# Optimization experiments

Hardware: AMD Instinct MI355X
Metric: run time of the kernel (lower is better)

Reference implementation:

```python
import jax, jax.numpy as jnp
import numpy as np

N = 100000   # nodes
E = 1600000  # edges (avg degree 16)
D = 128      # feature / hidden dim


def setup_inputs() -> dict:
    key = jax.random.key(0)
    k_x, k_e, k_w1, k_w2 = jax.random.split(key, 4)
    scale = 1.0 / np.sqrt(D)
    return {
        "x": jax.random.normal(k_x, (N, D), dtype=jnp.float32),
        "W1": jax.random.normal(k_w1, (D, D), dtype=jnp.float32) * scale,
        "b1": jnp.zeros((D,), dtype=jnp.float32),
        "W2": jax.random.normal(k_w2, (D, D), dtype=jnp.float32) * scale,
        "b2": jnp.zeros((D,), dtype=jnp.float32),
        "edge_index": jax.random.randint(k_e, (2, E), 0, N, dtype=jnp.int64),
    }


def _gcn_conv(h, src, dst, norm, W, b, n_nodes):
    # GCNConv: out = scatter_add(norm * (h @ W)[src] -> dst) + b
    y = h @ W                                   # [N, D] dense GEMM
    msgs = y[src] * norm[:, None]               # [E+N, D] gather + scale
    agg = jax.ops.segment_sum(msgs, dst, num_segments=n_nodes)  # scatter-add
    return agg + b


def reference(x, W1, b1, W2, b2, edge_index):
    n_nodes = x.shape[0]
    # add self loops (GCNConv default add_self_loops=True)
    loop = jnp.arange(n_nodes, dtype=edge_index.dtype)
    src = jnp.concatenate([edge_index[0], loop])
    dst = jnp.concatenate([edge_index[1], loop])
    # symmetric normalization: deg over destinations incl. self loops
    deg = jax.ops.segment_sum(jnp.ones_like(src, dtype=x.dtype), dst,
                              num_segments=n_nodes)
    dinv = jnp.where(deg > 0, jax.lax.rsqrt(deg), 0.0)
    norm = dinv[src] * dinv[dst]                # [E+N]
    # dropout in eval mode (identity); layer = conv -> ReLU, twice
    h = jax.nn.relu(_gcn_conv(x, src, dst, norm, W1, b1, n_nodes))
    h = jax.nn.relu(_gcn_conv(h, src, dst, norm, W2, b2, n_nodes))
    return h
```

## Files before the change

kernel.cpp:

```cpp
#include <hip/hip_runtime.h>
#include <hip/hip_bf16.h>


#define DIM 128
#define BSH 9
#define NBKT 196

typedef __attribute__((ext_vector_type(8))) short bf16x8;
typedef __attribute__((ext_vector_type(4))) float f32x4;


__global__ __launch_bounds__(256) void k_bcount(const int* __restrict__ dst,
                                                int E, int* __restrict__ bcnt) {
    __shared__ int h[NBKT];
    int t = threadIdx.x;
    for (int b = t; b < NBKT; b += 256) h[b] = 0;
    __syncthreads();
    for (int e = blockIdx.x * 256 + t; e < E; e += gridDim.x * 256)
        atomicAdd(&h[dst[e] >> BSH], 1);
    __syncthreads();
    for (int b = t; b < NBKT; b += 256)
        if (h[b]) atomicAdd(&bcnt[b], h[b]);
}

__global__ void k_bscan(const int* __restrict__ bcnt, int* __restrict__ bbase,
                        int* __restrict__ bcur) {
    __shared__ int a[256], c[256];
    int t = threadIdx.x;
    int v = (t < NBKT) ? bcnt[t] : 0;
    a[t] = v;
    __syncthreads();
    int* A = a; int* B = c;
    for (int off = 1; off < 256; off <<= 1) {
        B[t] = A[t] + (t >= off ? A[t - off] : 0);
        __syncthreads();
        int* tmp = A; A = B; B = tmp;
    }
    int incl = A[t];
    if (t < NBKT) { int ex = incl - v; bbase[t] = ex; bcur[t] = ex; }
    if (t == NBKT - 1) bbase[NBKT] = incl;
}

__global__ __launch_bounds__(256) void k_bscatter(
    const int* __restrict__ src, const int* __restrict__ dst, int E,
    int* __restrict__ bcur, uint2* __restrict__ out) {
    __shared__ uint2 stage[NBKT * 16];
    __shared__ int scnt[NBKT];
    __shared__ int needflush;
    int t = threadIdx.x;
    for (int b = t; b < NBKT; b += 256) scnt[b] = 0;
    if (t == 0) needflush = 0;
    __syncthreads();

    int per = (E + gridDim.x - 1) / gridDim.x;
    int s0 = blockIdx.x * per;
    int s1 = min(E, s0 + per);

    for (int base = s0; base < s1; base += 1024) {
#pragma unroll
        for (int k = 0; k < 4; ++k) {
            int e = base + t + k * 256;
            if (e < s1) {
                int d = dst[e];
                uint2 pr; pr.x = (uint)d; pr.y = (uint)src[e];
                int b = d >> BSH;
                int slot = atomicAdd(&scnt[b], 1);
                if (slot < 16) {
                    stage[b * 16 + slot] = pr;
                    if (slot == 15) needflush = 1;
                } else {
                    int c = atomicAdd(&bcur[b], 1);
                    out[c] = pr;
                }
            }
        }
        __syncthreads();
        if (needflush) {
            for (int bb = t; bb < NBKT; bb += 256) {
                if (scnt[bb] >= 16) {
                    int cur = atomicAdd(&bcur[bb], 16);
#pragma unroll
                    for (int k = 0; k < 16; ++k) out[cur + k] = stage[bb * 16 + k];
                    scnt[bb] = 0;
                }
            }
            __syncthreads();
            if (t == 0) needflush = 0;
            __syncthreads();
        }
    }
    for (int bb = t; bb < NBKT; bb += 256) {
        int c = scnt[bb]; if (c > 16) c = 16;
        if (c > 0) {
            int cur = atomicAdd(&bcur[bb], c);
            for (int k = 0; k < c; ++k) out[cur + k] = stage[bb * 16 + k];
        }
    }
}

__global__ __launch_bounds__(256) void k_bcsc(
    const uint2* __restrict__ pairs, const int* __restrict__ bbase,
    int* __restrict__ rowptr, float* __restrict__ dinv,
    int* __restrict__ col, int n) {
    __shared__ int lh[512], ls[512];
    int b = blockIdx.x, t = threadIdx.x;
    int p0 = bbase[b], p1 = bbase[b + 1];
    int d0 = b << BSH;

    lh[t] = 0; lh[t + 256] = 0;
    __syncthreads();
    for (int i = p0 + t; i < p1; i += 256)
        atomicAdd(&lh[pairs[i].x & 511], 1);
    __syncthreads();

    int deg0 = lh[t], deg1 = lh[t + 256];
    int* A = lh; int* B = ls;
    for (int off = 1; off < 512; off <<= 1) {
        B[t]       = A[t]       + (t       >= off ? A[t - off]       : 0);
        B[t + 256] = A[t + 256] + (t + 256 >= off ? A[t + 256 - off] : 0);
        __syncthreads();
        int* tmp = A; A = B; B = tmp;
    }
    int ex0 = A[t] - deg0, ex1 = A[t + 256] - deg1;
    __syncthreads();
    B[t] = ex0; B[t + 256] = ex1;

    int nd = d0 + t;
    if (nd < n) { rowptr[nd] = p0 + ex0; dinv[nd] = rsqrtf((float)(deg0 + 1)); }
    nd = d0 + t + 256;
    if (nd < n) { rowptr[nd] = p0 + ex1; dinv[nd] = rsqrtf((float)(deg1 + 1)); }
    if (b == NBKT - 1 && t == 0) rowptr[n] = p1;
    __syncthreads();

    for (int i = p0 + t; i < p1; i += 256) {
        uint2 pr = pairs[i];
        int slot = p0 + atomicAdd(&B[pr.x & 511], 1);
        col[slot] = (int)pr.y;
    }
}


__global__ void k_cast_x(const float* __restrict__ x, ushort* __restrict__ xb,
                         int total4) {
    int i = blockIdx.x * 256 + threadIdx.x;
    if (i < total4) {
        float4 v = ((const float4*)x)[i];
        __hip_bfloat16 a = __float2bfloat16(v.x), b = __float2bfloat16(v.y);
        __hip_bfloat16 c = __float2bfloat16(v.z), d = __float2bfloat16(v.w);
        ushort4 o = make_ushort4(*(ushort*)&a, *(ushort*)&b,
                                 *(ushort*)&c, *(ushort*)&d);
        ((ushort4*)xb)[i] = o;
    }
}

__global__ void k_split_w(const float* __restrict__ W, ushort* __restrict__ Wpk) {
    int idx = blockIdx.x * 256 + threadIdx.x;
    if (idx >= 16384) return;
    int j    = idx & 7;
    int lane = (idx >> 3) & 63;
    int ks   = (idx >> 9) & 3;
    int ct   = idx >> 11;
    int k  = ks * 32 + (lane >> 4) * 8 + j;
    int nn = ct * 16 + (lane & 15);
    float w = W[k * 128 + nn];
    __hip_bfloat16 hi = __float2bfloat16(w);
    float rem = w - __bfloat162float(hi);
    __hip_bfloat16 lo = __float2bfloat16(rem);
    Wpk[idx]         = *(ushort*)&hi;
    Wpk[16384 + idx] = *(ushort*)&lo;
}

__global__ __launch_bounds__(256, 2) void k_gemm_mfma(
    const ushort* __restrict__ xb, const ushort* __restrict__ Wpk,
    const float* __restrict__ dinv, ushort* __restrict__ y,
    int n, int ntiles) {
    __shared__ ushort Wl[32768];
    int t = threadIdx.x;
    {
        const uint4* s4 = (const uint4*)Wpk;
        uint4* d4 = (uint4*)Wl;
#pragma unroll
        for (int i = 0; i < 16; ++i) d4[t + 256 * i] = s4[t + 256 * i];
    }
    __syncthreads();

    const int wave = t >> 6, lane = t & 63;
    const int l15 = lane & 15, lg = lane >> 4;

    for (int tile = blockIdx.x; tile < ntiles; tile += gridDim.x) {
        int row0 = tile * 64 + wave * 16;
        int arow = row0 + l15;
        if (arow >= n) arow = n - 1;
        const ushort* xp = xb + (size_t)arow * 128 + lg * 8;

        bf16x8 a[4];
#pragma unroll
        for (int ks = 0; ks < 4; ++ks)
            a[ks] = *(const bf16x8*)(xp + ks * 32);

        f32x4 acc[8];
#pragma unroll
        for (int ct = 0; ct < 8; ++ct) acc[ct] = (f32x4)(0.f);

#pragma unroll
        for (int ks = 0; ks < 4; ++ks) {
#pragma unroll
            for (int ct = 0; ct < 8; ++ct) {
                bf16x8 b = *(const bf16x8*)&Wl[(size_t)((0 * 8 + ct) * 4 + ks) * 512 + lane * 8];
                acc[ct] = __builtin_amdgcn_mfma_f32_16x16x32_bf16(a[ks], b, acc[ct], 0, 0, 0);
            }
#pragma unroll
            for (int ct = 0; ct < 8; ++ct) {
                bf16x8 b = *(const bf16x8*)&Wl[(size_t)((1 * 8 + ct) * 4 + ks) * 512 + lane * 8];
                acc[ct] = __builtin_amdgcn_mfma_f32_16x16x32_bf16(a[ks], b, acc[ct], 0, 0, 0);
            }
        }

#pragma unroll
        for (int r = 0; r < 4; ++r) {
            int row = row0 + lg * 4 + r;
            if (row < n) {
                float dv = dinv[row];
                ushort* yr = y + (size_t)row * 128 + l15;
#pragma unroll
                for (int ct = 0; ct < 8; ++ct) {
                    __hip_bfloat16 h = __float2bfloat16(acc[ct][r] * dv);
                    yr[ct * 16] = *(ushort*)&h;
                }
            }
        }
    }
}

template <int MODE>
__global__ __launch_bounds__(256) void k_agg2(
    const ushort* __restrict__ yb, const int* __restrict__ rowptr,
    const int* __restrict__ col, const float* __restrict__ dinv,
    const float* __restrict__ bias, void* __restrict__ outp, int n) {
    int t = threadIdx.x, lane = t & 63;
    int node = blockIdx.x * 4 + (t >> 6);
    if (node >= n) return;

    uint v0 = *(const uint*)(yb + (size_t)node * 128 + lane * 2);
    float ax = __uint_as_float(v0 << 16);
    float ay = __uint_as_float(v0 & 0xffff0000u);

    int lo = rowptr[node], hi = rowptr[node + 1];
    int i = lo;
    for (; i + 4 <= hi; i += 4) {
        int s0 = col[i], s1 = col[i + 1], s2 = col[i + 2], s3 = col[i + 3];
        uint w0 = *(const uint*)(yb + (size_t)s0 * 128 + lane * 2);
        uint w1 = *(const uint*)(yb + (size_t)s1 * 128 + lane * 2);
        uint w2 = *(const uint*)(yb + (size_t)s2 * 128 + lane * 2);
        uint w3 = *(const uint*)(yb + (size_t)s3 * 128 + lane * 2);
        ax += __uint_as_float(w0 << 16);         ay += __uint_as_float(w0 & 0xffff0000u);
        ax += __uint_as_float(w1 << 16);         ay += __uint_as_float(w1 & 0xffff0000u);
        ax += __uint_as_float(w2 << 16);         ay += __uint_as_float(w2 & 0xffff0000u);
        ax += __uint_as_float(w3 << 16);         ay += __uint_as_float(w3 & 0xffff0000u);
    }
    for (; i < hi; ++i) {
        int s = col[i];
        uint w = *(const uint*)(yb + (size_t)s * 128 + lane * 2);
        ax += __uint_as_float(w << 16);
        ay += __uint_as_float(w & 0xffff0000u);
    }

    float dv = dinv[node];
    float2 b = ((const float2*)bias)[lane];
    float ox = fmaxf(ax * dv + b.x, 0.f);
    float oy = fmaxf(ay * dv + b.y, 0.f);

    if (MODE == 0) {
        __hip_bfloat16 ha = __float2bfloat16(ox), hb = __float2bfloat16(oy);
        uint o = ((uint)(*(ushort*)&hb) << 16) | (uint)(*(ushort*)&ha);
        ((uint*)outp)[(size_t)node * 64 + lane] = o;
    } else {
        ((float2*)outp)[(size_t)node * 64 + lane] = make_float2(ox, oy);
    }
}


extern "C" void kernel_launch(void* const* d_in, const int* in_sizes, int n_in,
                              void* d_out, int out_size, void* d_ws, size_t ws_size,
                              hipStream_t stream) {
    const float* x  = (const float*)d_in[0];
    const float* W1 = (const float*)d_in[1];
    const float* b1 = (const float*)d_in[2];
    const float* W2 = (const float*)d_in[3];
    const float* b2 = (const float*)d_in[4];
    const int*   ei = (const int*)d_in[5];

    const int n = in_sizes[0] / DIM;
    const int E = in_sizes[5] / 2;
    const int* src = ei;
    const int* dst = ei + E;
    float* out = (float*)d_out;

    char* w = (char*)d_ws;
    ushort* xb    = (ushort*)w;  w += (size_t)n * DIM * sizeof(ushort);
    ushort* h     = (ushort*)w;  w += (size_t)n * DIM * sizeof(ushort);
    uint2*  bpair = (uint2*)w;   w += (size_t)E * sizeof(uint2);
    ushort* wpk1  = (ushort*)w;  w += 32768 * sizeof(ushort);
    ushort* wpk2  = (ushort*)w;  w += 32768 * sizeof(ushort);
    float*  dinv  = (float*)w;   w += (size_t)n * sizeof(float);
    int*    rowptr= (int*)w;     w += (size_t)(n + 4) * sizeof(int);
    int*    col   = (int*)w;     w += (size_t)E * sizeof(int);
    int*    bcnt  = (int*)w;     w += NBKT * sizeof(int);
    int*    bbase = (int*)w;     w += (NBKT + 4) * sizeof(int);
    int*    bcur  = (int*)w;     w += NBKT * sizeof(int);

    ushort* y = xb;

    const int nbAgg  = (n + 3) / 4;
    const int ntiles = (n + 63) / 64;
    const int nbGemm = 512;
    const int nbCast = (n * DIM / 4 + 255) / 256;

    hipMemsetAsync(bcnt, 0, NBKT * sizeof(int), stream);
    k_bcount  <<<256,  256, 0, stream>>>(dst, E, bcnt);
    k_bscan   <<<1,    256, 0, stream>>>(bcnt, bbase, bcur);
    k_bscatter<<<768,  256, 0, stream>>>(src, dst, E, bcur, bpair);
    k_bcsc    <<<NBKT, 256, 0, stream>>>(bpair, bbase, rowptr, dinv, col, n);

    k_split_w<<<64, 256, 0, stream>>>(W1, wpk1);
    k_split_w<<<64, 256, 0, stream>>>(W2, wpk2);
    k_cast_x<<<nbCast, 256, 0, stream>>>(x, xb, n * DIM / 4);

    k_gemm_mfma<<<nbGemm, 256, 0, stream>>>(xb, wpk1, dinv, y, n, ntiles);
    k_agg2<0><<<nbAgg, 256, 0, stream>>>(y, rowptr, col, dinv, b1, h, n);

    k_gemm_mfma<<<nbGemm, 256, 0, stream>>>(h, wpk2, dinv, y, n, ntiles);
    k_agg2<1><<<nbAgg, 256, 0, stream>>>(y, rowptr, col, dinv, b2, out, n);
}
```

Before: 428.3 us.

## Fuse x cast into GEMM, pack edge pairs, merge weight split, deepen gather unroll

The separate fp32-to-bf16 cast kernel for x is removed; the first GEMM now reads fp32 x and converts in registers. Edge pairs are packed into one 32-bit word (9-bit local dst, 17-bit src), which halves scatter and CSR-build traffic and doubles the LDS staging depth. The two weight-split launches become one. The aggregation loop now issues 8 gathers at once and makes the node index wave-uniform. The packing assumes src fits in 17 bits, so it only holds for n up to 131072.

After: 371.0 us. 13.4% less time.

```diff
diff --git a/kernel.cpp b/kernel.cpp
--- a/kernel.cpp
+++ b/kernel.cpp
@@ -8,6 +8,11 @@
 
 typedef __attribute__((ext_vector_type(8))) short bf16x8;
 typedef __attribute__((ext_vector_type(4))) float f32x4;
+
+static __device__ __forceinline__ ushort bfbits(float f) {
+    __hip_bfloat16 h = __float2bfloat16(f);
+    return *(ushort*)&h;
+}
 
 
 __global__ __launch_bounds__(256) void k_bcount(const int* __restrict__ dst,
@@ -43,8 +48,8 @@
 
 __global__ __launch_bounds__(256) void k_bscatter(
     const int* __restrict__ src, const int* __restrict__ dst, int E,
-    int* __restrict__ bcur, uint2* __restrict__ out) {
-    __shared__ uint2 stage[NBKT * 16];
+    int* __restrict__ bcur, uint* __restrict__ out) {
+    __shared__ uint stage[NBKT * 32];
     __shared__ int scnt[NBKT];
     __shared__ int needflush;
     int t = threadIdx.x;
@@ -62,12 +67,12 @@
             int e = base + t + k * 256;
             if (e < s1) {
                 int d = dst[e];
-                uint2 pr; pr.x = (uint)d; pr.y = (uint)src[e];
+                uint pr = ((uint)(d & 511) << 17) | (uint)src[e];
                 int b = d >> BSH;
                 int slot = atomicAdd(&scnt[b], 1);
-                if (slot < 16) {
-                    stage[b * 16 + slot] = pr;
-                    if (slot == 15) needflush = 1;
+                if (slot < 32) {
+                    stage[b * 32 + slot] = pr;
+                    if (slot == 31) needflush = 1;
                 } else {
                     int c = atomicAdd(&bcur[b], 1);
                     out[c] = pr;
@@ -77,10 +82,10 @@
         __syncthreads();
         if (needflush) {
             for (int bb = t; bb < NBKT; bb += 256) {
-                if (scnt[bb] >= 16) {
-                    int cur = atomicAdd(&bcur[bb], 16);
-#pragma unroll
-                    for (int k = 0; k < 16; ++k) out[cur + k] = stage[bb * 16 + k];
+                if (scnt[bb] >= 32) {
+                    int cur = atomicAdd(&bcur[bb], 32);
+#pragma unroll
+                    for (int k = 0; k < 32; ++k) out[cur + k] = stage[bb * 32 + k];
                     scnt[bb] = 0;
                 }
             }
@@ -90,16 +95,16 @@
         }
     }
     for (int bb = t; bb < NBKT; bb += 256) {
-        int c = scnt[bb]; if (c > 16) c = 16;
+        int c = scnt[bb]; if (c > 32) c = 32;
         if (c > 0) {
             int cur = atomicAdd(&bcur[bb], c);
-            for (int k = 0; k < c; ++k) out[cur + k] = stage[bb * 16 + k];
+            for (int k = 0; k < c; ++k) out[cur + k] = stage[bb * 32 + k];
         }
     }
 }
 
 __global__ __launch_bounds__(256) void k_bcsc(
-    const uint2* __restrict__ pairs, const int* __restrict__ bbase,
+    const uint* __restrict__ pairs, const int* __restrict__ bbase,
     int* __restrict__ rowptr, float* __restrict__ dinv,
     int* __restrict__ col, int n) {
     __shared__ int lh[512], ls[512];
@@ -110,7 +115,7 @@
     lh[t] = 0; lh[t + 256] = 0;
     __syncthreads();
     for (int i = p0 + t; i < p1; i += 256)
-        atomicAdd(&lh[pairs[i].x & 511], 1);
+        atomicAdd(&lh[pairs[i] >> 17], 1);
     __syncthreads();
 
     int deg0 = lh[t], deg1 = lh[t + 256];
@@ -133,29 +138,20 @@
     __syncthreads();
 
     for (int i = p0 + t; i < p1; i += 256) {
-        uint2 pr = pairs[i];
-        int slot = p0 + atomicAdd(&B[pr.x & 511], 1);
-        col[slot] = (int)pr.y;
-    }
-}
-
-
-__global__ void k_cast_x(const float* __restrict__ x, ushort* __restrict__ xb,
-                         int total4) {
-    int i = blockIdx.x * 256 + threadIdx.x;
-    if (i < total4) {
-        float4 v = ((const float4*)x)[i];
-        __hip_bfloat16 a = __float2bfloat16(v.x), b = __float2bfloat16(v.y);
-        __hip_bfloat16 c = __float2bfloat16(v.z), d = __float2bfloat16(v.w);
-        ushort4 o = make_ushort4(*(ushort*)&a, *(ushort*)&b,
-                                 *(ushort*)&c, *(ushort*)&d);
-        ((ushort4*)xb)[i] = o;
-    }
-}
-
-__global__ void k_split_w(const float* __restrict__ W, ushort* __restrict__ Wpk) {
-    int idx = blockIdx.x * 256 + threadIdx.x;
-    if (idx >= 16384) return;
+        uint pr = pairs[i];
+        int slot = p0 + atomicAdd(&B[pr >> 17], 1);
+        col[slot] = (int)(pr & 0x1FFFFu);
+    }
+}
+
+__global__ void k_split_w2(const float* __restrict__ W1,
+                           const float* __restrict__ W2,
+                           ushort* __restrict__ wpk1,
+                           ushort* __restrict__ wpk2) {
+    int g = blockIdx.x;
+    const float* W   = (g < 64) ? W1 : W2;
+    ushort* Wpk      = (g < 64) ? wpk1 : wpk2;
+    int idx = (g & 63) * 256 + threadIdx.x;
     int j    = idx & 7;
     int lane = (idx >> 3) & 63;
     int ks   = (idx >> 9) & 3;
@@ -165,13 +161,13 @@
     float w = W[k * 128 + nn];
     __hip_bfloat16 hi = __float2bfloat16(w);
     float rem = w - __bfloat162float(hi);
-    __hip_bfloat16 lo = __float2bfloat16(rem);
     Wpk[idx]         = *(ushort*)&hi;
-    Wpk[16384 + idx] = *(ushort*)&lo;
-}
-
+    Wpk[16384 + idx] = bfbits(rem);
+}
+
+template <int INF32>
 __global__ __launch_bounds__(256, 2) void k_gemm_mfma(
-    const ushort* __restrict__ xb, const ushort* __restrict__ Wpk,
+    const void* __restrict__ xin, const ushort* __restrict__ Wpk,
     const float* __restrict__ dinv, ushort* __restrict__ y,
     int n, int ntiles) {
     __shared__ ushort Wl[32768];
@@ -191,12 +187,27 @@
         int row0 = tile * 64 + wave * 16;
         int arow = row0 + l15;
         if (arow >= n) arow = n - 1;
-        const ushort* xp = xb + (size_t)arow * 128 + lg * 8;
 
         bf16x8 a[4];
-#pragma unroll
-        for (int ks = 0; ks < 4; ++ks)
-            a[ks] = *(const bf16x8*)(xp + ks * 32);
+        if (INF32) {
+            const float* xp = (const float*)xin + (size_t)arow * 128 + lg * 8;
+#pragma unroll
+            for (int ks = 0; ks < 4; ++ks) {
+                float4 f0 = *(const float4*)(xp + ks * 32);
+                float4 f1 = *(const float4*)(xp + ks * 32 + 4);
+                bf16x8 av;
+                av[0] = (short)bfbits(f0.x); av[1] = (short)bfbits(f0.y);
+                av[2] = (short)bfbits(f0.z); av[3] = (short)bfbits(f0.w);
+                av[4] = (short)bfbits(f1.x); av[5] = (short)bfbits(f1.y);
+                av[6] = (short)bfbits(f1.z); av[7] = (short)bfbits(f1.w);
+                a[ks] = av;
+            }
+        } else {
+            const ushort* xp = (const ushort*)xin + (size_t)arow * 128 + lg * 8;
+#pragma unroll
+            for (int ks = 0; ks < 4; ++ks)
+                a[ks] = *(const bf16x8*)(xp + ks * 32);
+        }
 
         f32x4 acc[8];
 #pragma unroll
@@ -223,10 +234,8 @@
                 float dv = dinv[row];
                 ushort* yr = y + (size_t)row * 128 + l15;
 #pragma unroll
-                for (int ct = 0; ct < 8; ++ct) {
-                    __hip_bfloat16 h = __float2bfloat16(acc[ct][r] * dv);
-                    yr[ct * 16] = *(ushort*)&h;
-                }
+                for (int ct = 0; ct < 8; ++ct)
+                    yr[ct * 16] = bfbits(acc[ct][r] * dv);
             }
         }
     }
@@ -238,7 +247,7 @@
     const int* __restrict__ col, const float* __restrict__ dinv,
     const float* __restrict__ bias, void* __restrict__ outp, int n) {
     int t = threadIdx.x, lane = t & 63;
-    int node = blockIdx.x * 4 + (t >> 6);
+    int node = __builtin_amdgcn_readfirstlane(blockIdx.x * 4 + (t >> 6));
     if (node >= n) return;
 
     uint v0 = *(const uint*)(yb + (size_t)node * 128 + lane * 2);
@@ -247,20 +256,30 @@
 
     int lo = rowptr[node], hi = rowptr[node + 1];
     int i = lo;
+    for (; i + 8 <= hi; i += 8) {
+        uint w[8];
+#pragma unroll
+        for (int k = 0; k < 8; ++k)
+            w[k] = *(const uint*)(yb + (size_t)col[i + k] * 128 + lane * 2);
+#pragma unroll
+        for (int k = 0; k < 8; ++k) {
+            ax += __uint_as_float(w[k] << 16);
+            ay += __uint_as_float(w[k] & 0xffff0000u);
+        }
+    }
     for (; i + 4 <= hi; i += 4) {
-        int s0 = col[i], s1 = col[i + 1], s2 = col[i + 2], s3 = col[i + 3];
-        uint w0 = *(const uint*)(yb + (size_t)s0 * 128 + lane * 2);
-        uint w1 = *(const uint*)(yb + (size_t)s1 * 128 + lane * 2);
-        uint w2 = *(const uint*)(yb + (size_t)s2 * 128 + lane * 2);
-        uint w3 = *(const uint*)(yb + (size_t)s3 * 128 + lane * 2);
-        ax += __uint_as_float(w0 << 16);         ay += __uint_as_float(w0 & 0xffff0000u);
-        ax += __uint_as_float(w1 << 16);         ay += __uint_as_float(w1 & 0xffff0000u);
-        ax += __uint_as_float(w2 << 16);         ay += __uint_as_float(w2 & 0xffff0000u);
-        ax += __uint_as_float(w3 << 16);         ay += __uint_as_float(w3 & 0xffff0000u);
+        uint w[4];
+#pragma unroll
+        for (int k = 0; k < 4; ++k)
+            w[k] = *(const uint*)(yb + (size_t)col[i + k] * 128 + lane * 2);
+#pragma unroll
+        for (int k = 0; k < 4; ++k) {
+            ax += __uint_as_float(w[k] << 16);
+            ay += __uint_as_float(w[k] & 0xffff0000u);
+        }
     }
     for (; i < hi; ++i) {
-        int s = col[i];
-        uint w = *(const uint*)(yb + (size_t)s * 128 + lane * 2);
+        uint w = *(const uint*)(yb + (size_t)col[i] * 128 + lane * 2);
         ax += __uint_as_float(w << 16);
         ay += __uint_as_float(w & 0xffff0000u);
     }
@@ -271,8 +290,7 @@
     float oy = fmaxf(ay * dv + b.y, 0.f);
 
     if (MODE == 0) {
-        __hip_bfloat16 ha = __float2bfloat16(ox), hb = __float2bfloat16(oy);
-        uint o = ((uint)(*(ushort*)&hb) << 16) | (uint)(*(ushort*)&ha);
+        uint o = ((uint)bfbits(oy) << 16) | (uint)bfbits(ox);
         ((uint*)outp)[(size_t)node * 64 + lane] = o;
     } else {
         ((float2*)outp)[(size_t)node * 64 + lane] = make_float2(ox, oy);
@@ -297,9 +315,9 @@
     float* out = (float*)d_out;
 
     char* w = (char*)d_ws;
-    ushort* xb    = (ushort*)w;  w += (size_t)n * DIM * sizeof(ushort);
+    ushort* y     = (ushort*)w;  w += (size_t)n * DIM * sizeof(ushort);
     ushort* h     = (ushort*)w;  w += (size_t)n * DIM * sizeof(ushort);
-    uint2*  bpair = (uint2*)w;   w += (size_t)E * sizeof(uint2);
+    uint*   bpair = (uint*)w;    w += (size_t)E * sizeof(uint);
     ushort* wpk1  = (ushort*)w;  w += 32768 * sizeof(ushort);
     ushort* wpk2  = (ushort*)w;  w += 32768 * sizeof(ushort);
     float*  dinv  = (float*)w;   w += (size_t)n * sizeof(float);
@@ -309,12 +327,9 @@
     int*    bbase = (int*)w;     w += (NBKT + 4) * sizeof(int);
     int*    bcur  = (int*)w;     w += NBKT * sizeof(int);
 
-    ushort* y = xb;
-
     const int nbAgg  = (n + 3) / 4;
     const int ntiles = (n + 63) / 64;
     const int nbGemm = 512;
-    const int nbCast = (n * DIM / 4 + 255) / 256;
 
     hipMemsetAsync(bcnt, 0, NBKT * sizeof(int), stream);
     k_bcount  <<<256,  256, 0, stream>>>(dst, E, bcnt);
@@ -322,13 +337,11 @@
     k_bscatter<<<768,  256, 0, stream>>>(src, dst, E, bcur, bpair);
     k_bcsc    <<<NBKT, 256, 0, stream>>>(bpair, bbase, rowptr, dinv, col, n);
 
-    k_split_w<<<64, 256, 0, stream>>>(W1, wpk1);
-    k_split_w<<<64, 256, 0, stream>>>(W2, wpk2);
-    k_cast_x<<<nbCast, 256, 0, stream>>>(x, xb, n * DIM / 4);
-
-    k_gemm_mfma<<<nbGemm, 256, 0, stream>>>(xb, wpk1, dinv, y, n, ntiles);
+    k_split_w2<<<128, 256, 0, stream>>>(W1, W2, wpk1, wpk2);
+
+    k_gemm_mfma<1><<<nbGemm, 256, 0, stream>>>(x, wpk1, dinv, y, n, ntiles);
     k_agg2<0><<<nbAgg, 256, 0, stream>>>(y, rowptr, col, dinv, b1, h, n);
 
-    k_gemm_mfma<<<nbGemm, 256, 0, stream>>>(h, wpk2, dinv, y, n, ntiles);
+    k_gemm_mfma<0><<<nbGemm, 256, 0, stream>>>(h, wpk2, dinv, y, n, ntiles);
     k_agg2<1><<<nbAgg, 256, 0, stream>>>(y, rowptr, col, dinv, b2, out, n);
 }
```
